# Optimization experiments

Measured on AMD Instinct MI355X. Metric: run time of the kernel, lower is better.

Reference implementation:

```python
import jax, jax.numpy as jnp
import numpy as np

WEIGHT_BITS = 8
INPUT_BITS = 8


def fake_quant(t, bits):
    """Per-tensor symmetric absmax fake quantization with straight-through estimator."""
    qmax = 2.0 ** (bits - 1) - 1.0  # e.g. 127 for 8 bits
    scale = jnp.maximum(jnp.max(jnp.abs(t)), 1e-8) / qmax
    q = jnp.round(t / scale) * scale
    return t + jax.lax.stop_gradient(q - t)


def setup_inputs() -> dict:
    key = jax.random.key(0)
    k0, k1, k2, k3 = jax.random.split(key, 4)
    d, f, n = 4096, 11008, 4096
    s_in = 1.0 / np.sqrt(d)
    s_ff = 1.0 / np.sqrt(f)
    return {
        "x": jax.random.normal(k0, (n, d), jnp.float32),
        "w1": jax.random.normal(k1, (f, d), jnp.float32) * s_in,  # fc1: embed -> ffn
        "w3": jax.random.normal(k2, (f, d), jnp.float32) * s_in,  # fc3: gate proj
        "w2": jax.random.normal(k3, (d, f), jnp.float32) * s_ff,  # fc2: ffn -> embed
    }


def reference(x, w1, w3, w2):
    # quantized fc3 -> silu gate
    xq = fake_quant(x, INPUT_BITS)
    gate = jax.nn.silu(jnp.einsum('nd,fd->nf', xq, fake_quant(w3, WEIGHT_BITS)))
    # quantized fc1, multiplied by gate (GLU)
    h = jnp.einsum('nd,fd->nf', xq, fake_quant(w1, WEIGHT_BITS)) * gate
    # subln=False -> no ffn_layernorm; dropout=0 (eval)
    hq = fake_quant(h, INPUT_BITS)
    out = jnp.einsum('nf,df->nd', hq, fake_quant(w2, WEIGHT_BITS))
    return out
```

## Files before the change

### kernel.cpp

```cpp
#include <hip/hip_runtime.h>
#include <hip/hip_bf16.h>

typedef __attribute__((ext_vector_type(4))) int int4v;

#define MFMA_I8(a, b, c) __builtin_amdgcn_mfma_i32_16x16x64_i8((a), (b), (c), 0, 0, 0)
#define GLDS16(g, l)                                                                        \
  __builtin_amdgcn_global_load_lds((const __attribute__((address_space(1))) void*)(g),      \
                                   (__attribute__((address_space(3))) void*)(l), 16, 0, 0)
#define SBAR() __builtin_amdgcn_s_barrier()
#define SCHED0() __builtin_amdgcn_sched_barrier(0)

static constexpr int NTOK = 4096;
static constexpr int DDIM = 4096;
static constexpr int FDIM = 11008;


__device__ __forceinline__ float wave_max64(float m) {
#pragma unroll
  for (int o = 32; o > 0; o >>= 1) m = fmaxf(m, __shfl_xor(m, o));
  return m;
}

__global__ void zero_slots(unsigned* s) {
  if (threadIdx.x < 16) s[threadIdx.x] = 0u;
}

__device__ __forceinline__ void absmax_body(const float* __restrict__ p, int n4,
                                            unsigned* __restrict__ slot) {
  float m = 0.f;
  const int stride = gridDim.x * blockDim.x;
  for (int i = blockIdx.x * blockDim.x + threadIdx.x; i < n4; i += stride) {
    float4 v = reinterpret_cast<const float4*>(p)[i];
    m = fmaxf(fmaxf(fabsf(v.x), fabsf(v.y)), fmaxf(fmaxf(fabsf(v.z), fabsf(v.w)), m));
  }
  m = wave_max64(m);
  __shared__ float wm[4];
  const int lane = threadIdx.x & 63, w = threadIdx.x >> 6;
  if (lane == 0) wm[w] = m;
  __syncthreads();
  if (threadIdx.x == 0) {
    m = fmaxf(fmaxf(wm[0], wm[1]), fmaxf(wm[2], wm[3]));
    atomicMax(slot, __float_as_uint(m));
  }
}

__global__ void absmax4(const float* x, const float* w1, const float* w3, const float* w2,
                        unsigned* slots, int n4x, int n4w) {
  const int seg = blockIdx.y;
  const float* p = (seg == 0) ? x : (seg == 1) ? w1 : (seg == 2) ? w3 : w2;
  absmax_body(p, seg == 0 ? n4x : n4w, slots + seg);
}

__device__ __forceinline__ void quant_body(const float* __restrict__ in,
                                           unsigned* __restrict__ out, int n4,
                                           const unsigned* __restrict__ slot) {
  const float s = fmaxf(__uint_as_float(*slot), 1e-8f) / 127.0f;
  const int stride = gridDim.x * blockDim.x;
  for (int i = blockIdx.x * blockDim.x + threadIdx.x; i < n4; i += stride) {
    float4 v = reinterpret_cast<const float4*>(in)[i];
    const int q0 = (int)rintf(v.x / s), q1 = (int)rintf(v.y / s);
    const int q2 = (int)rintf(v.z / s), q3 = (int)rintf(v.w / s);
    out[i] = (unsigned)(q0 & 255) | ((unsigned)(q1 & 255) << 8) |
             ((unsigned)(q2 & 255) << 16) | ((unsigned)(q3 & 255) << 24);
  }
}

__device__ __forceinline__ void quantW_frag_body(const float* __restrict__ in,
                                                 int4v* __restrict__ out,
                                                 const unsigned* __restrict__ slot,
                                                 int K, int NKT, int total) {
  const float s = fmaxf(__uint_as_float(*slot), 1e-8f) / 127.0f;
  const int stride = gridDim.x * blockDim.x;
  for (int u = blockIdx.x * blockDim.x + threadIdx.x; u < total; u += stride) {
    const int block = u >> 8;
    const int sidx = u & 255;
    const int fi = sidx >> 6;
    const int l = sidx & 63;
    const int p = block / NKT;
    const int kt = block - p * NKT;
    const int row = p * 32 + (fi & 1) * 16 + (l & 15);
    const int k0 = kt * 128 + (fi >> 1) * 64 + (l >> 4) * 16;
    const float4* src = reinterpret_cast<const float4*>(in + (size_t)row * K + k0);
    unsigned r[4];
#pragma unroll
    for (int j = 0; j < 4; ++j) {
      float4 v = src[j];
      const int q0 = (int)rintf(v.x / s), q1 = (int)rintf(v.y / s);
      const int q2 = (int)rintf(v.z / s), q3 = (int)rintf(v.w / s);
      r[j] = (unsigned)(q0 & 255) | ((unsigned)(q1 & 255) << 8) |
             ((unsigned)(q2 & 255) << 16) | ((unsigned)(q3 & 255) << 24);
    }
    out[u] = (int4v){(int)r[0], (int)r[1], (int)r[2], (int)r[3]};
  }
}

__global__ void quant4(const float* x, const float* w1, const float* w3, const float* w2,
                       unsigned* qx, unsigned* qw1, unsigned* qw3, unsigned* qw2,
                       const unsigned* slots, int n4x, int n4w) {
  const int seg = blockIdx.y;
  const int totW = FDIM * (DDIM / 16);
  if (seg == 0) quant_body(x, qx, n4x, slots + 0);
  else if (seg == 1) quantW_frag_body(w1, (int4v*)qw1, slots + 1, DDIM, DDIM / 128, totW);
  else if (seg == 2) quantW_frag_body(w3, (int4v*)qw3, slots + 2, DDIM, DDIM / 128, totW);
  else quantW_frag_body(w2, (int4v*)qw2, slots + 3, FDIM, FDIM / 128, totW);
}

__global__ void quant_kernel(const float* __restrict__ in, unsigned* __restrict__ out,
                             int n4, const unsigned* __restrict__ slot) {
  quant_body(in, out, n4, slot);
}

__global__ __launch_bounds__(256, 2) void gemm_glu(
    const signed char* __restrict__ Aq, const signed char* __restrict__ B3f,
    const signed char* __restrict__ B1f, float* __restrict__ H,
    const unsigned* __restrict__ slots, unsigned* __restrict__ hslot) {
  constexpr int K = DDIM;
  constexpr int NT = K >> 7;
  __shared__ char lds[32768];

  const int t = threadIdx.x;
  const int l = t & 63;
  const int w = t >> 6;

  const int gx = gridDim.x, gy = gridDim.y;
  const int nwg = gx * gy;
  const int i0 = blockIdx.y * gx + blockIdx.x;
  const int cid = (i0 & 7) * (nwg >> 3) + (i0 >> 3);
  const int rowA0 = (cid % gy) << 7;
  const int colB0 = (cid / gy) << 7;

  const int rlA = t >> 3;
  const int glA = (t & 7) ^ (rlA & 7);
  const signed char* aP = Aq + (size_t)(rowA0 + rlA) * K + glA * 16;
  const size_t r32 = (size_t)32 * K;
  const int stW = w * 1024;

  const int p0 = (colB0 >> 5) + w;
  const signed char* w3b = B3f + (size_t)p0 * 32 * 4096 + l * 16;
  const signed char* w1b = B1f + (size_t)p0 * 32 * 4096 + l * 16;

#define STAGE_A(KT, BUF)                                   \
  do {                                                     \
    const size_t kO_ = (size_t)(KT) * 128;                 \
    GLDS16(aP + kO_, &lds[(BUF) + stW]);                   \
    GLDS16(aP + r32 + kO_, &lds[(BUF) + 4096 + stW]);      \
    GLDS16(aP + 2 * r32 + kO_, &lds[(BUF) + 8192 + stW]);  \
    GLDS16(aP + 3 * r32 + kO_, &lds[(BUF) + 12288 + stW]); \
  } while (0)

#define LDSF(BASE, R, G)                                                      \
  (*reinterpret_cast<const int4v*>(                                           \
      &lds[(BASE) + (R)*128 + (((G) ^ ((R)&7)) << 4)]))

  int4v acc3[8][2], acc1[8][2];
#pragma unroll
  for (int m = 0; m < 8; ++m)
#pragma unroll
    for (int n = 0; n < 2; ++n) {
      acc3[m][n] = (int4v){0, 0, 0, 0};
      acc1[m][n] = (int4v){0, 0, 0, 0};
    }

  const int lr = l & 15;
  const int cr = l >> 4;

  int4v b3k0[2], b3k1[2], b1k0[2], b1k1[2];

  STAGE_A(0, 0);
  {
    b3k0[0] = *(const int4v*)(w3b);
    b3k0[1] = *(const int4v*)(w3b + 1024);
    b3k1[0] = *(const int4v*)(w3b + 2048);
    b3k1[1] = *(const int4v*)(w3b + 3072);
    b1k0[0] = *(const int4v*)(w1b);
    b1k0[1] = *(const int4v*)(w1b + 1024);
    b1k1[0] = *(const int4v*)(w1b + 2048);
    b1k1[1] = *(const int4v*)(w1b + 3072);
  }

  for (int kt = 0; kt < NT; ++kt) {
    const int rb = (kt & 1) * 16384;
    const bool nx = (kt + 1 < NT);
    const signed char* p3n = w3b + (size_t)(kt + 1) * 4096;
    const signed char* p1n = w1b + (size_t)(kt + 1) * 4096;

    SCHED0();
    asm volatile("s_waitcnt vmcnt(8)" ::: "memory");
    SBAR();
    SCHED0();

    if (nx) STAGE_A(kt + 1, rb ^ 16384);

    int4v a_[8];
#pragma unroll
    for (int m = 0; m < 8; ++m) a_[m] = LDSF(rb, m * 16 + lr, cr);
    __builtin_amdgcn_s_setprio(1);
#pragma unroll
    for (int m = 0; m < 8; ++m) {
      acc3[m][0] = MFMA_I8(a_[m], b3k0[0], acc3[m][0]);
      acc3[m][1] = MFMA_I8(a_[m], b3k0[1], acc3[m][1]);
      acc1[m][0] = MFMA_I8(a_[m], b1k0[0], acc1[m][0]);
      acc1[m][1] = MFMA_I8(a_[m], b1k0[1], acc1[m][1]);
    }
    __builtin_amdgcn_s_setprio(0);

    if (nx) {
      b3k0[0] = *(const int4v*)(p3n);
      b3k0[1] = *(const int4v*)(p3n + 1024);
      b1k0[0] = *(const int4v*)(p1n);
      b1k0[1] = *(const int4v*)(p1n + 1024);
    }

#pragma unroll
    for (int m = 0; m < 8; ++m) a_[m] = LDSF(rb, m * 16 + lr, 4 + cr);
    __builtin_amdgcn_s_setprio(1);
#pragma unroll
    for (int m = 0; m < 8; ++m) {
      acc3[m][0] = MFMA_I8(a_[m], b3k1[0], acc3[m][0]);
      acc3[m][1] = MFMA_I8(a_[m], b3k1[1], acc3[m][1]);
      acc1[m][0] = MFMA_I8(a_[m], b1k1[0], acc1[m][0]);
      acc1[m][1] = MFMA_I8(a_[m], b1k1[1], acc1[m][1]);
    }
    __builtin_amdgcn_s_setprio(0);

    if (nx) {
      b3k1[0] = *(const int4v*)(p3n + 2048);
      b3k1[1] = *(const int4v*)(p3n + 3072);
      b1k1[0] = *(const int4v*)(p1n + 2048);
      b1k1[1] = *(const int4v*)(p1n + 3072);
    }
  }

  const float sx = fmaxf(__uint_as_float(slots[0]), 1e-8f) / 127.0f;
  const float sw1 = fmaxf(__uint_as_float(slots[1]), 1e-8f) / 127.0f;
  const float sw3 = fmaxf(__uint_as_float(slots[2]), 1e-8f) / 127.0f;
  const float s3 = sx * sw3, s1 = sx * sw1;
  const int crow0 = rowA0 + ((l >> 4) << 2);
  const int ccol0 = colB0 + w * 32 + lr;
  float hmax = 0.f;
#pragma unroll
  for (int m = 0; m < 8; ++m)
#pragma unroll
    for (int n = 0; n < 2; ++n)
#pragma unroll
      for (int j = 0; j < 4; ++j) {
        const int row = crow0 + m * 16 + j;
        const int col = ccol0 + n * 16;
        const float g = (float)acc3[m][n][j] * s3;
        const float gate = g / (1.f + expf(-g));
        const float h = (float)acc1[m][n][j] * s1 * gate;
        H[(size_t)row * FDIM + col] = h;
        hmax = fmaxf(hmax, fabsf(h));
      }
  hmax = wave_max64(hmax);
  if (l == 0) atomicMax(hslot, __float_as_uint(hmax));
#undef STAGE_A
#undef LDSF
}

__global__ __launch_bounds__(256, 3) void gemm_down(
    const signed char* __restrict__ Aq, const signed char* __restrict__ B2f,
    float* __restrict__ C, const unsigned* __restrict__ slots) {
  constexpr int K = FDIM;
  constexpr int NT = K >> 7;
  constexpr int NKT = K >> 7;
  __shared__ char lds[32768];

  const int t = threadIdx.x;
  const int l = t & 63;
  const int w = t >> 6;

  const int gx = gridDim.x, gy = gridDim.y;
  const int nwg = gx * gy;
  const int i0 = blockIdx.y * gx + blockIdx.x;
  const int cid = (i0 & 7) * (nwg >> 3) + (i0 >> 3);
  const int rowA0 = (cid % gy) << 7;
  const int colB0 = (cid / gy) << 7;

  const int rlA = t >> 3;
  const int glA = (t & 7) ^ (rlA & 7);
  const signed char* aP = Aq + (size_t)(rowA0 + rlA) * K + glA * 16;
  const size_t r32 = (size_t)32 * K;
  const int stW = w * 1024;

  const int p0 = (colB0 >> 5) + w;
  const signed char* w2b = B2f + (size_t)p0 * NKT * 4096 + l * 16;

#define STAGE_A(KT, BUF)                                   \
  do {                                                     \
    const size_t kO_ = (size_t)(KT) * 128;                 \
    GLDS16(aP + kO_, &lds[(BUF) + stW]);                   \
    GLDS16(aP + r32 + kO_, &lds[(BUF) + 4096 + stW]);      \
    GLDS16(aP + 2 * r32 + kO_, &lds[(BUF) + 8192 + stW]);  \
    GLDS16(aP + 3 * r32 + kO_, &lds[(BUF) + 12288 + stW]); \
  } while (0)

#define LDSF(BASE, R, G)                                                      \
  (*reinterpret_cast<const int4v*>(                                           \
      &lds[(BASE) + (R)*128 + (((G) ^ ((R)&7)) << 4)]))

  int4v acc[8][2];
#pragma unroll
  for (int m = 0; m < 8; ++m)
#pragma unroll
    for (int n = 0; n < 2; ++n) acc[m][n] = (int4v){0, 0, 0, 0};

  const int lr = l & 15;
  const int cr = l >> 4;

  int4v bk0[2], bk1[2];

  STAGE_A(0, 0);
  bk0[0] = *(const int4v*)(w2b);
  bk0[1] = *(const int4v*)(w2b + 1024);
  bk1[0] = *(const int4v*)(w2b + 2048);
  bk1[1] = *(const int4v*)(w2b + 3072);

  for (int kt = 0; kt < NT; ++kt) {
    const int rb = (kt & 1) * 16384;
    const bool nx = (kt + 1 < NT);
    const signed char* pn = w2b + (size_t)(kt + 1) * 4096;

    SCHED0();
    asm volatile("s_waitcnt vmcnt(4)" ::: "memory");
    SBAR();
    SCHED0();

    if (nx) STAGE_A(kt + 1, rb ^ 16384);

    int4v a_[8];
#pragma unroll
    for (int m = 0; m < 8; ++m) a_[m] = LDSF(rb, m * 16 + lr, cr);
    __builtin_amdgcn_s_setprio(1);
#pragma unroll
    for (int m = 0; m < 8; ++m) {
      acc[m][0] = MFMA_I8(a_[m], bk0[0], acc[m][0]);
      acc[m][1] = MFMA_I8(a_[m], bk0[1], acc[m][1]);
    }
    __builtin_amdgcn_s_setprio(0);

    if (nx) {
      bk0[0] = *(const int4v*)(pn);
      bk0[1] = *(const int4v*)(pn + 1024);
    }

#pragma unroll
    for (int m = 0; m < 8; ++m) a_[m] = LDSF(rb, m * 16 + lr, 4 + cr);
    __builtin_amdgcn_s_setprio(1);
#pragma unroll
    for (int m = 0; m < 8; ++m) {
      acc[m][0] = MFMA_I8(a_[m], bk1[0], acc[m][0]);
      acc[m][1] = MFMA_I8(a_[m], bk1[1], acc[m][1]);
    }
    __builtin_amdgcn_s_setprio(0);

    if (nx) {
      bk1[0] = *(const int4v*)(pn + 2048);
      bk1[1] = *(const int4v*)(pn + 3072);
    }
  }

  const float sa = fmaxf(__uint_as_float(slots[4]), 1e-8f) / 127.0f;
  const float sb = fmaxf(__uint_as_float(slots[3]), 1e-8f) / 127.0f;
  const float s = sa * sb;
  const int crow0 = rowA0 + ((l >> 4) << 2);
  const int ccol0 = colB0 + w * 32 + lr;
#pragma unroll
  for (int m = 0; m < 8; ++m)
#pragma unroll
    for (int n = 0; n < 2; ++n)
#pragma unroll
      for (int j = 0; j < 4; ++j) {
        const int row = crow0 + m * 16 + j;
        const int col = ccol0 + n * 16;
        C[(size_t)row * DDIM + col] = (float)acc[m][n][j] * s;
      }
#undef STAGE_A
#undef LDSF
}


extern "C" void kernel_launch(void* const* d_in, const int* in_sizes, int n_in,
                              void* d_out, int out_size, void* d_ws, size_t ws_size,
                              hipStream_t stream) {
  const float* x = (const float*)d_in[0];
  const float* w1 = (const float*)d_in[1];
  const float* w3 = (const float*)d_in[2];
  const float* w2 = (const float*)d_in[3];
  float* out = (float*)d_out;
  char* ws = (char*)d_ws;

  unsigned* slots = (unsigned*)ws;
  size_t off = 256;
  signed char* qx = (signed char*)(ws + off);
  off += (size_t)NTOK * DDIM;
  signed char* qw3 = (signed char*)(ws + off);
  off += (size_t)FDIM * DDIM;
  signed char* qw1 = (signed char*)(ws + off);
  off += (size_t)FDIM * DDIM;
  signed char* qw2 = (signed char*)(ws + off);
  off += (size_t)FDIM * DDIM;
  float* H = (float*)(ws + off);
  off += (size_t)NTOK * FDIM * 4;
  signed char* qh = (signed char*)(ws + off);
  off += (size_t)NTOK * FDIM;

  const int n4x = NTOK * DDIM / 4;
  const int n4w = FDIM * DDIM / 4;
  const int n4h = NTOK * FDIM / 4;

  zero_slots<<<1, 64, 0, stream>>>(slots);
  absmax4<<<dim3(512, 4), 256, 0, stream>>>(x, w1, w3, w2, slots, n4x, n4w);
  quant4<<<dim3(2048, 4), 256, 0, stream>>>(x, w1, w3, w2, (unsigned*)qx, (unsigned*)qw1,
                                            (unsigned*)qw3, (unsigned*)qw2, slots, n4x, n4w);

  const dim3 gGlu(FDIM / 128, NTOK / 128);
  gemm_glu<<<gGlu, 256, 0, stream>>>(qx, qw3, qw1, H, slots, slots + 4);
  quant_kernel<<<2048, 256, 0, stream>>>(H, (unsigned*)qh, n4h, slots + 4);
  const dim3 gDn(DDIM / 128, NTOK / 128);
  gemm_down<<<gDn, 256, 0, stream>>>(qh, qw2, out, slots);
}
```

Before: 894.3 us.

## Switch GEMM wave tiling from 128x32 to 2x2 grid of 64x64 tiles

Both int8 GEMM kernels change per-wave tiling from one wave covering all 128 rows by 32 columns to a 2x2 wave grid, each wave covering 64x64. This halves the LDS A-fragment reads per wave while doubling the B fragments each wave loads directly from global memory, which rebalances LDS traffic against global and register traffic. Wait counts are adjusted to match the larger number of in-flight B loads. Each wave now holds more live B registers, which could add register pressure in the two-GEMM GLU kernel.

```diff
diff --git a/kernel.cpp b/kernel.cpp
--- a/kernel.cpp
+++ b/kernel.cpp
@@ -116,11 +116,14 @@
     const unsigned* __restrict__ slots, unsigned* __restrict__ hslot) {
   constexpr int K = DDIM;
   constexpr int NT = K >> 7;
+  constexpr int NKT = K >> 7;
   __shared__ char lds[32768];
 
   const int t = threadIdx.x;
   const int l = t & 63;
   const int w = t >> 6;
+  const int wm = w >> 1;
+  const int wn = w & 1;
 
   const int gx = gridDim.x, gy = gridDim.y;
   const int nwg = gx * gy;
@@ -135,9 +138,11 @@
   const size_t r32 = (size_t)32 * K;
   const int stW = w * 1024;
 
-  const int p0 = (colB0 >> 5) + w;
-  const signed char* w3b = B3f + (size_t)p0 * 32 * 4096 + l * 16;
-  const signed char* w1b = B1f + (size_t)p0 * 32 * 4096 + l * 16;
+  const int pA = (colB0 >> 5) + wn * 2;
+  const signed char* b3p0 = B3f + (size_t)pA * NKT * 4096 + l * 16;
+  const signed char* b3p1 = b3p0 + (size_t)NKT * 4096;
+  const signed char* b1p0 = B1f + (size_t)pA * NKT * 4096 + l * 16;
+  const signed char* b1p1 = b1p0 + (size_t)NKT * 4096;
 
 #define STAGE_A(KT, BUF)                                   \
   do {                                                     \
@@ -152,96 +157,92 @@
   (*reinterpret_cast<const int4v*>(                                           \
       &lds[(BASE) + (R)*128 + (((G) ^ ((R)&7)) << 4)]))
 
-  int4v acc3[8][2], acc1[8][2];
-#pragma unroll
-  for (int m = 0; m < 8; ++m)
-#pragma unroll
-    for (int n = 0; n < 2; ++n) {
+#define LOADB_KK(KT, KK, B3A, B1A)                                   \
+  do {                                                               \
+    const size_t o_ = (size_t)(KT)*4096 + (KK)*2048;                 \
+    B3A[KK][0] = *(const int4v*)(b3p0 + o_);                         \
+    B3A[KK][1] = *(const int4v*)(b3p0 + o_ + 1024);                  \
+    B3A[KK][2] = *(const int4v*)(b3p1 + o_);                         \
+    B3A[KK][3] = *(const int4v*)(b3p1 + o_ + 1024);                  \
+    B1A[KK][0] = *(const int4v*)(b1p0 + o_);                         \
+    B1A[KK][1] = *(const int4v*)(b1p0 + o_ + 1024);                  \
+    B1A[KK][2] = *(const int4v*)(b1p1 + o_);                         \
+    B1A[KK][3] = *(const int4v*)(b1p1 + o_ + 1024);                  \
+  } while (0)
+
+  int4v acc3[4][4], acc1[4][4];
+#pragma unroll
+  for (int m = 0; m < 4; ++m)
+#pragma unroll
+    for (int n = 0; n < 4; ++n) {
       acc3[m][n] = (int4v){0, 0, 0, 0};
       acc1[m][n] = (int4v){0, 0, 0, 0};
     }
 
   const int lr = l & 15;
   const int cr = l >> 4;
-
-  int4v b3k0[2], b3k1[2], b1k0[2], b1k1[2];
+  const int ar0 = wm * 64 + lr;
+
+  int4v b3[2][4], b1[2][4];
 
   STAGE_A(0, 0);
-  {
-    b3k0[0] = *(const int4v*)(w3b);
-    b3k0[1] = *(const int4v*)(w3b + 1024);
-    b3k1[0] = *(const int4v*)(w3b + 2048);
-    b3k1[1] = *(const int4v*)(w3b + 3072);
-    b1k0[0] = *(const int4v*)(w1b);
-    b1k0[1] = *(const int4v*)(w1b + 1024);
-    b1k1[0] = *(const int4v*)(w1b + 2048);
-    b1k1[1] = *(const int4v*)(w1b + 3072);
-  }
+  LOADB_KK(0, 0, b3, b1);
+  LOADB_KK(0, 1, b3, b1);
 
   for (int kt = 0; kt < NT; ++kt) {
     const int rb = (kt & 1) * 16384;
     const bool nx = (kt + 1 < NT);
-    const signed char* p3n = w3b + (size_t)(kt + 1) * 4096;
-    const signed char* p1n = w1b + (size_t)(kt + 1) * 4096;
 
     SCHED0();
-    asm volatile("s_waitcnt vmcnt(8)" ::: "memory");
+    if (nx) {
+      asm volatile("s_waitcnt vmcnt(16)" ::: "memory");
+    } else {
+      asm volatile("s_waitcnt vmcnt(0)" ::: "memory");
+    }
     SBAR();
     SCHED0();
 
     if (nx) STAGE_A(kt + 1, rb ^ 16384);
 
-    int4v a_[8];
-#pragma unroll
-    for (int m = 0; m < 8; ++m) a_[m] = LDSF(rb, m * 16 + lr, cr);
+    int4v a_[4];
+#pragma unroll
+    for (int m = 0; m < 4; ++m) a_[m] = LDSF(rb, ar0 + m * 16, cr);
     __builtin_amdgcn_s_setprio(1);
 #pragma unroll
-    for (int m = 0; m < 8; ++m) {
-      acc3[m][0] = MFMA_I8(a_[m], b3k0[0], acc3[m][0]);
-      acc3[m][1] = MFMA_I8(a_[m], b3k0[1], acc3[m][1]);
-      acc1[m][0] = MFMA_I8(a_[m], b1k0[0], acc1[m][0]);
-      acc1[m][1] = MFMA_I8(a_[m], b1k0[1], acc1[m][1]);
-    }
+    for (int m = 0; m < 4; ++m)
+#pragma unroll
+      for (int n = 0; n < 4; ++n) {
+        acc3[m][n] = MFMA_I8(a_[m], b3[0][n], acc3[m][n]);
+        acc1[m][n] = MFMA_I8(a_[m], b1[0][n], acc1[m][n]);
+      }
     __builtin_amdgcn_s_setprio(0);
-
-    if (nx) {
-      b3k0[0] = *(const int4v*)(p3n);
-      b3k0[1] = *(const int4v*)(p3n + 1024);
-      b1k0[0] = *(const int4v*)(p1n);
-      b1k0[1] = *(const int4v*)(p1n + 1024);
-    }
-
-#pragma unroll
-    for (int m = 0; m < 8; ++m) a_[m] = LDSF(rb, m * 16 + lr, 4 + cr);
+    if (nx) LOADB_KK(kt + 1, 0, b3, b1);
+
+#pragma unroll
+    for (int m = 0; m < 4; ++m) a_[m] = LDSF(rb, ar0 + m * 16, 4 + cr);
     __builtin_amdgcn_s_setprio(1);
 #pragma unroll
-    for (int m = 0; m < 8; ++m) {
-      acc3[m][0] = MFMA_I8(a_[m], b3k1[0], acc3[m][0]);
-      acc3[m][1] = MFMA_I8(a_[m], b3k1[1], acc3[m][1]);
-      acc1[m][0] = MFMA_I8(a_[m], b1k1[0], acc1[m][0]);
-      acc1[m][1] = MFMA_I8(a_[m], b1k1[1], acc1[m][1]);
-    }
+    for (int m = 0; m < 4; ++m)
+#pragma unroll
+      for (int n = 0; n < 4; ++n) {
+        acc3[m][n] = MFMA_I8(a_[m], b3[1][n], acc3[m][n]);
+        acc1[m][n] = MFMA_I8(a_[m], b1[1][n], acc1[m][n]);
+      }
     __builtin_amdgcn_s_setprio(0);
-
-    if (nx) {
-      b3k1[0] = *(const int4v*)(p3n + 2048);
-      b3k1[1] = *(const int4v*)(p3n + 3072);
-      b1k1[0] = *(const int4v*)(p1n + 2048);
-      b1k1[1] = *(const int4v*)(p1n + 3072);
-    }
+    if (nx) LOADB_KK(kt + 1, 1, b3, b1);
   }
 
   const float sx = fmaxf(__uint_as_float(slots[0]), 1e-8f) / 127.0f;
   const float sw1 = fmaxf(__uint_as_float(slots[1]), 1e-8f) / 127.0f;
   const float sw3 = fmaxf(__uint_as_float(slots[2]), 1e-8f) / 127.0f;
   const float s3 = sx * sw3, s1 = sx * sw1;
-  const int crow0 = rowA0 + ((l >> 4) << 2);
-  const int ccol0 = colB0 + w * 32 + lr;
+  const int crow0 = rowA0 + wm * 64 + ((l >> 4) << 2);
+  const int ccol0 = colB0 + wn * 64 + lr;
   float hmax = 0.f;
 #pragma unroll
-  for (int m = 0; m < 8; ++m)
-#pragma unroll
-    for (int n = 0; n < 2; ++n)
+  for (int m = 0; m < 4; ++m)
+#pragma unroll
+    for (int n = 0; n < 4; ++n)
 #pragma unroll
       for (int j = 0; j < 4; ++j) {
         const int row = crow0 + m * 16 + j;
@@ -256,6 +257,7 @@
   if (l == 0) atomicMax(hslot, __float_as_uint(hmax));
 #undef STAGE_A
 #undef LDSF
+#undef LOADB_KK
 }
 
 __global__ __launch_bounds__(256, 3) void gemm_down(
@@ -269,6 +271,8 @@
   const int t = threadIdx.x;
   const int l = t & 63;
   const int w = t >> 6;
+  const int wm = w >> 1;
+  const int wn = w & 1;
 
   const int gx = gridDim.x, gy = gridDim.y;
   const int nwg = gx * gy;
@@ -283,8 +287,9 @@
   const size_t r32 = (size_t)32 * K;
   const int stW = w * 1024;
 
-  const int p0 = (colB0 >> 5) + w;
-  const signed char* w2b = B2f + (size_t)p0 * NKT * 4096 + l * 16;
+  const int pA = (colB0 >> 5) + wn * 2;
+  const signed char* b2p0 = B2f + (size_t)pA * NKT * 4096 + l * 16;
+  const signed char* b2p1 = b2p0 + (size_t)NKT * 4096;
 
 #define STAGE_A(KT, BUF)                                   \
   do {                                                     \
@@ -299,76 +304,77 @@
   (*reinterpret_cast<const int4v*>(                                           \
       &lds[(BASE) + (R)*128 + (((G) ^ ((R)&7)) << 4)]))
 
-  int4v acc[8][2];
-#pragma unroll
-  for (int m = 0; m < 8; ++m)
-#pragma unroll
-    for (int n = 0; n < 2; ++n) acc[m][n] = (int4v){0, 0, 0, 0};
+#define LOADB_KK(KT, KK, BA)                                         \
+  do {                                                               \
+    const size_t o_ = (size_t)(KT)*4096 + (KK)*2048;                 \
+    BA[KK][0] = *(const int4v*)(b2p0 + o_);                          \
+    BA[KK][1] = *(const int4v*)(b2p0 + o_ + 1024);                   \
+    BA[KK][2] = *(const int4v*)(b2p1 + o_);                          \
+    BA[KK][3] = *(const int4v*)(b2p1 + o_ + 1024);                   \
+  } while (0)
+
+  int4v acc[4][4];
+#pragma unroll
+  for (int m = 0; m < 4; ++m)
+#pragma unroll
+    for (int n = 0; n < 4; ++n) acc[m][n] = (int4v){0, 0, 0, 0};
 
   const int lr = l & 15;
   const int cr = l >> 4;
-
-  int4v bk0[2], bk1[2];
+  const int ar0 = wm * 64 + lr;
+
+  int4v b2[2][4];
 
   STAGE_A(0, 0);
-  bk0[0] = *(const int4v*)(w2b);
-  bk0[1] = *(const int4v*)(w2b + 1024);
-  bk1[0] = *(const int4v*)(w2b + 2048);
-  bk1[1] = *(const int4v*)(w2b + 3072);
+  LOADB_KK(0, 0, b2);
+  LOADB_KK(0, 1, b2);
 
   for (int kt = 0; kt < NT; ++kt) {
     const int rb = (kt & 1) * 16384;
     const bool nx = (kt + 1 < NT);
-    const signed char* pn = w2b + (size_t)(kt + 1) * 4096;
 
     SCHED0();
-    asm volatile("s_waitcnt vmcnt(4)" ::: "memory");
+    if (nx) {
+      asm volatile("s_waitcnt vmcnt(8)" ::: "memory");
+    } else {
+      asm volatile("s_waitcnt vmcnt(0)" ::: "memory");
+    }
     SBAR();
     SCHED0();
 
     if (nx) STAGE_A(kt + 1, rb ^ 16384);
 
-    int4v a_[8];
-#pragma unroll
-    for (int m = 0; m < 8; ++m) a_[m] = LDSF(rb, m * 16 + lr, cr);
+    int4v a_[4];
+#pragma unroll
+    for (int m = 0; m < 4; ++m) a_[m] = LDSF(rb, ar0 + m * 16, cr);
     __builtin_amdgcn_s_setprio(1);
 #pragma unroll
-    for (int m = 0; m < 8; ++m) {
-      acc[m][0] = MFMA_I8(a_[m], bk0[0], acc[m][0]);
-      acc[m][1] = MFMA_I8(a_[m], bk0[1], acc[m][1]);
-    }
+    for (int m = 0; m < 4; ++m)
+#pragma unroll
+      for (int n = 0; n < 4; ++n) acc[m][n] = MFMA_I8(a_[m], b2[0][n], acc[m][n]);
     __builtin_amdgcn_s_setprio(0);
-
-    if (nx) {
-      bk0[0] = *(const int4v*)(pn);
-      bk0[1] = *(const int4v*)(pn + 1024);
-    }
-
-#pragma unroll
-    for (int m = 0; m < 8; ++m) a_[m] = LDSF(rb, m * 16 + lr, 4 + cr);
+    if (nx) LOADB_KK(kt + 1, 0, b2);
+
+#pragma unroll
+    for (int m = 0; m < 4; ++m) a_[m] = LDSF(rb, ar0 + m * 16, 4 + cr);
     __builtin_amdgcn_s_setprio(1);
 #pragma unroll
-    for (int m = 0; m < 8; ++m) {
-      acc[m][0] = MFMA_I8(a_[m], bk1[0], acc[m][0]);
-      acc[m][1] = MFMA_I8(a_[m], bk1[1], acc[m][1]);
-    }
+    for (int m = 0; m < 4; ++m)
+#pragma unroll
+      for (int n = 0; n < 4; ++n) acc[m][n] = MFMA_I8(a_[m], b2[1][n], acc[m][n]);
     __builtin_amdgcn_s_setprio(0);
-
-    if (nx) {
-      bk1[0] = *(const int4v*)(pn + 2048);
-      bk1[1] = *(const int4v*)(pn + 3072);
-    }
+    if (nx) LOADB_KK(kt + 1, 1, b2);
   }
 
   const float sa = fmaxf(__uint_as_float(slots[4]), 1e-8f) / 127.0f;
   const float sb = fmaxf(__uint_as_float(slots[3]), 1e-8f) / 127.0f;
   const float s = sa * sb;
-  const int crow0 = rowA0 + ((l >> 4) << 2);
-  const int ccol0 = colB0 + w * 32 + lr;
-#pragma unroll
-  for (int m = 0; m < 8; ++m)
-#pragma unroll
-    for (int n = 0; n < 2; ++n)
+  const int crow0 = rowA0 + wm * 64 + ((l >> 4) << 2);
+  const int ccol0 = colB0 + wn * 64 + lr;
+#pragma unroll
+  for (int m = 0; m < 4; ++m)
+#pragma unroll
+    for (int n = 0; n < 4; ++n)
 #pragma unroll
       for (int j = 0; j < 4; ++j) {
         const int row = crow0 + m * 16 + j;
@@ -377,6 +383,7 @@
       }
 #undef STAGE_A
 #undef LDSF
+#undef LOADB_KK
 }
 
 
```

Result: slower. 956.0 us (+6.9%).
